# Kernel optimization log

Hardware: AMD Instinct MI355X
Metric: run time of the kernel (lower is better)

The kernel has to match this reference:

```python
import jax, jax.numpy as jnp
import numpy as np

ALPHA = 1.0
BETA = 0.5

B, N, E = 4096, 4096, 16384


def setup_inputs() -> dict:
    key = jax.random.key(0)
    k1, k2, k3, k4, k5 = jax.random.split(key, 5)
    outputs = jax.random.normal(k1, (B, N), dtype=jnp.float32)
    targets = jax.random.uniform(k2, (B, N), dtype=jnp.float32)
    # per-node level weight (equivalent to node_levels dict -> level_weights lookup)
    level_w = jax.random.uniform(k3, (N,), dtype=jnp.float32)
    edge_src = jax.random.randint(k4, (E,), 0, N, dtype=jnp.int32)  # parent i
    edge_dst = jax.random.randint(k5, (E,), 0, N, dtype=jnp.int32)  # child  j
    return {"outputs": outputs, "targets": targets, "level_w": level_w,
            "edge_src": edge_src, "edge_dst": edge_dst}


def reference(outputs, targets, level_w, edge_src, edge_dst):
    # BCEWithLogits, reduction='none': softplus(x) - x*t (numerically stable)
    bce = jax.nn.softplus(outputs) - outputs * targets          # [B, N]
    weighted_bce = bce * level_w[None, :]                        # [B, N]

    probs = jax.nn.sigmoid(outputs)                              # [B, N]
    # for each edge (i=parent, j=child): consistency[:, j] += relu(p[:, j] - p[:, i])
    diff = jax.nn.relu(probs[:, edge_dst] - probs[:, edge_src])  # [B, E]
    consistency = jnp.zeros_like(probs).at[:, edge_dst].add(diff)  # [B, N]

    return ALPHA * weighted_bce.mean() + BETA * consistency.mean()
```

## Files before the change

kernel.cpp:

```cpp
#include <hip/hip_runtime.h>
#include <math.h>


#define ALPHA_C 1.0f
#define BETA_C  0.5f

constexpr int B = 4096;
constexpr int N = 4096;
constexpr int E = 16384;
constexpr int THREADS = 1024;
constexpr int GRID = 256;
constexpr int R = 4;
constexpr int ROWS_PB = B / GRID;
constexpr int GPB = ROWS_PB / R;
constexpr int EPC = E / 4 / THREADS;

typedef _Float16 h4 __attribute__((ext_vector_type(4)));

__global__ __launch_bounds__(64) void init_out_kernel(float* out) {
    if (threadIdx.x == 0) out[0] = 0.0f;
}

__device__ __forceinline__ void fast_sig_sp(float x, float& p, float& sp) {
    float q = __expf(-fabsf(x));
    float d = 1.0f + q;
    float r = __builtin_amdgcn_rcpf(d);
    p  = (x >= 0.0f) ? r : q * r;
    sp = fmaxf(x, 0.0f) + __logf(d);
}

__global__ __launch_bounds__(THREADS, 4) void hier_loss_kernel(
    const float* __restrict__ outputs,
    const float* __restrict__ targets,
    const float* __restrict__ level_w,
    const int*   __restrict__ edge_src,
    const int*   __restrict__ edge_dst,
    float*       __restrict__ out)
{
    __shared__ h4 P[2][N];

    const int tid  = threadIdx.x;
    const int row0 = blockIdx.x * ROWS_PB;

    const float4* out4 = (const float4*)outputs;
    const float4* tgt4 = (const float4*)targets;
    const float4* lw4  = (const float4*)level_w;
    const int4*   es4  = (const int4*)edge_src;
    const int4*   ed4  = (const int4*)edge_dst;

    const float4 w = lw4[tid];
    const float wv[4] = {w.x, w.y, w.z, w.w};

    int4 se[EPC], de[EPC];
#pragma unroll
    for (int j = 0; j < EPC; ++j) {
        se[j] = es4[tid + j * THREADS];
        de[j] = ed4[tid + j * THREADS];
    }

    float s1 = 0.0f, s2 = 0.0f;
    float4 xs[R], ts[R];

#pragma unroll
    for (int r = 0; r < R; ++r) {
        const size_t idx = (size_t)(row0 + r) * (N / 4) + tid;
        xs[r] = out4[idx];
        ts[r] = tgt4[idx];
    }
    {
        h4 tmp[4];
#pragma unroll
        for (int r = 0; r < R; ++r) {
            const float xv[4] = {xs[r].x, xs[r].y, xs[r].z, xs[r].w};
            const float tv[4] = {ts[r].x, ts[r].y, ts[r].z, ts[r].w};
#pragma unroll
            for (int k = 0; k < 4; ++k) {
                float p, sp;
                fast_sig_sp(xv[k], p, sp);
                s1 = fmaf(wv[k], sp - xv[k] * tv[k], s1);
                tmp[k][r] = (_Float16)p;
            }
        }
#pragma unroll
        for (int k = 0; k < 4; ++k) P[0][4 * tid + k] = tmp[k];
    }
    __syncthreads();

#pragma unroll
    for (int kg = 0; kg < GPB; ++kg) {
        if (kg + 1 < GPB) {
#pragma unroll
            for (int r = 0; r < R; ++r) {
                const size_t idx = (size_t)(row0 + (kg + 1) * R + r) * (N / 4) + tid;
                xs[r] = out4[idx];
                ts[r] = tgt4[idx];
            }
        }
        __builtin_amdgcn_sched_barrier(0);

        {
            const h4* Pc = P[kg & 1];
            h4 acc0 = {0, 0, 0, 0};
            h4 acc1 = {0, 0, 0, 0};
            const h4 zero = {0, 0, 0, 0};
#pragma unroll
            for (int j = 0; j < EPC; ++j) {
                const int4 s = se[j];
                const int4 d = de[j];
                h4 a0 = Pc[s.x], c0 = Pc[d.x];
                h4 a1 = Pc[s.y], c1 = Pc[d.y];
                h4 a2 = Pc[s.z], c2 = Pc[d.z];
                h4 a3 = Pc[s.w], c3 = Pc[d.w];
                acc0 += __builtin_elementwise_max(c0 - a0, zero);
                acc1 += __builtin_elementwise_max(c1 - a1, zero);
                acc0 += __builtin_elementwise_max(c2 - a2, zero);
                acc1 += __builtin_elementwise_max(c3 - a3, zero);
            }
#pragma unroll
            for (int l = 0; l < 4; ++l) s2 += (float)acc0[l] + (float)acc1[l];
        }
        __builtin_amdgcn_sched_barrier(0);

        if (kg + 1 < GPB) {
            h4 tmp[4];
#pragma unroll
            for (int r = 0; r < R; ++r) {
                const float xv[4] = {xs[r].x, xs[r].y, xs[r].z, xs[r].w};
                const float tv[4] = {ts[r].x, ts[r].y, ts[r].z, ts[r].w};
#pragma unroll
                for (int k = 0; k < 4; ++k) {
                    float p, sp;
                    fast_sig_sp(xv[k], p, sp);
                    s1 = fmaf(wv[k], sp - xv[k] * tv[k], s1);
                    tmp[k][r] = (_Float16)p;
                }
            }
#pragma unroll
            for (int k = 0; k < 4; ++k) P[(kg + 1) & 1][4 * tid + k] = tmp[k];
        }
        __syncthreads();
    }

#pragma unroll
    for (int off = 32; off > 0; off >>= 1) {
        s1 += __shfl_down(s1, off, 64);
        s2 += __shfl_down(s2, off, 64);
    }
    float* red = (float*)P;
    const int wave = tid >> 6;
    const int lane = tid & 63;
    if (lane == 0) { red[wave] = s1; red[16 + wave] = s2; }
    __syncthreads();
    if (tid == 0) {
        float a = 0.0f, c = 0.0f;
#pragma unroll
        for (int v = 0; v < 16; ++v) { a += red[v]; c += red[16 + v]; }
        const float inv = 1.0f / ((float)B * (float)N);
        atomicAdd(out, (ALPHA_C * a + BETA_C * c) * inv);
    }
}

extern "C" void kernel_launch(void* const* d_in, const int* in_sizes, int n_in,
                              void* d_out, int out_size, void* d_ws, size_t ws_size,
                              hipStream_t stream) {
    const float* outputs = (const float*)d_in[0];
    const float* targets = (const float*)d_in[1];
    const float* level_w = (const float*)d_in[2];
    const int*   edge_src = (const int*)d_in[3];
    const int*   edge_dst = (const int*)d_in[4];
    float* out = (float*)d_out;

    init_out_kernel<<<1, 64, 0, stream>>>(out);
    hier_loss_kernel<<<GRID, THREADS, 0, stream>>>(outputs, targets, level_w,
                                                   edge_src, edge_dst, out);
}
```

Measured before the change: 155.1 us.

## Prefetch two row groups ahead and stage edge indices in LDS as u16

Deepens the global-load prefetch from one to two row groups by double-buffering the input registers. Edge indices move from per-thread registers into shared memory as 16-bit values, freeing VGPRs at the cost of extra LDS reads per edge batch. The __syncthreads calls become a manual lgkmcnt wait plus s_barrier so the barrier does not wait on outstanding global loads. The deeper prefetch and larger LDS footprint may reduce occupancy.

Result: slower. 160.3 us (+3.4%).

```diff
diff --git a/kernel.cpp b/kernel.cpp
--- a/kernel.cpp
+++ b/kernel.cpp
@@ -13,9 +13,10 @@
 constexpr int R = 4;
 constexpr int ROWS_PB = B / GRID;
 constexpr int GPB = ROWS_PB / R;
-constexpr int EPC = E / 4 / THREADS;
+constexpr int EPT4 = E / 4 / THREADS;
 
 typedef _Float16 h4 __attribute__((ext_vector_type(4)));
+typedef unsigned short us4 __attribute__((ext_vector_type(4)));
 
 __global__ __launch_bounds__(64) void init_out_kernel(float* out) {
     if (threadIdx.x == 0) out[0] = 0.0f;
@@ -38,6 +39,8 @@
     float*       __restrict__ out)
 {
     __shared__ h4 P[2][N];
+    __shared__ unsigned short IS[E];
+    __shared__ unsigned short ID[E];
 
     const int tid  = threadIdx.x;
     const int row0 = blockIdx.x * ROWS_PB;
@@ -47,32 +50,50 @@
     const float4* lw4  = (const float4*)level_w;
     const int4*   es4  = (const int4*)edge_src;
     const int4*   ed4  = (const int4*)edge_dst;
+    us4* IS4 = (us4*)IS;
+    us4* ID4 = (us4*)ID;
+
+    float s1 = 0.0f, s2 = 0.0f;
 
     const float4 w = lw4[tid];
+    int4 sei[EPT4], dei[EPT4];
+#pragma unroll
+    for (int j = 0; j < EPT4; ++j) {
+        sei[j] = es4[tid + j * THREADS];
+        dei[j] = ed4[tid + j * THREADS];
+    }
+    float4 xs[2][R], ts[2][R];
+#pragma unroll
+    for (int g = 0; g < 2; ++g)
+#pragma unroll
+    for (int r = 0; r < R; ++r) {
+        const size_t idx = (size_t)(row0 + g * R + r) * (N / 4) + tid;
+        xs[g][r] = out4[idx];
+        ts[g][r] = tgt4[idx];
+    }
+    __builtin_amdgcn_sched_barrier(0);
+
     const float wv[4] = {w.x, w.y, w.z, w.w};
 
-    int4 se[EPC], de[EPC];
 #pragma unroll
-    for (int j = 0; j < EPC; ++j) {
-        se[j] = es4[tid + j * THREADS];
-        de[j] = ed4[tid + j * THREADS];
+    for (int j = 0; j < EPT4; ++j) {
+        us4 ps = {(unsigned short)sei[j].x, (unsigned short)sei[j].y,
+                  (unsigned short)sei[j].z, (unsigned short)sei[j].w};
+        us4 pd = {(unsigned short)dei[j].x, (unsigned short)dei[j].y,
+                  (unsigned short)dei[j].z, (unsigned short)dei[j].w};
+        IS4[tid + j * THREADS] = ps;
+        ID4[tid + j * THREADS] = pd;
     }
+    __builtin_amdgcn_sched_barrier(0);
 
-    float s1 = 0.0f, s2 = 0.0f;
-    float4 xs[R], ts[R];
-
-#pragma unroll
-    for (int r = 0; r < R; ++r) {
-        const size_t idx = (size_t)(row0 + r) * (N / 4) + tid;
-        xs[r] = out4[idx];
-        ts[r] = tgt4[idx];
-    }
-    {
+    auto transform = [&](int slot, h4* Pb) {
         h4 tmp[4];
 #pragma unroll
         for (int r = 0; r < R; ++r) {
-            const float xv[4] = {xs[r].x, xs[r].y, xs[r].z, xs[r].w};
-            const float tv[4] = {ts[r].x, ts[r].y, ts[r].z, ts[r].w};
+            const float xv[4] = {xs[slot][r].x, xs[slot][r].y,
+                                 xs[slot][r].z, xs[slot][r].w};
+            const float tv[4] = {ts[slot][r].x, ts[slot][r].y,
+                                 ts[slot][r].z, ts[slot][r].w};
 #pragma unroll
             for (int k = 0; k < 4; ++k) {
                 float p, sp;
@@ -82,18 +103,24 @@
             }
         }
 #pragma unroll
-        for (int k = 0; k < 4; ++k) P[0][4 * tid + k] = tmp[k];
-    }
-    __syncthreads();
+        for (int k = 0; k < 4; ++k) Pb[4 * tid + k] = tmp[k];
+    };
+
+    transform(0, P[0]);
+    asm volatile("s_waitcnt lgkmcnt(0)" ::: "memory");
+    __builtin_amdgcn_s_barrier();
+    __builtin_amdgcn_sched_barrier(0);
 
 #pragma unroll
     for (int kg = 0; kg < GPB; ++kg) {
-        if (kg + 1 < GPB) {
+        if (kg + 2 < GPB) {
+            const int slot = kg & 1;
 #pragma unroll
             for (int r = 0; r < R; ++r) {
-                const size_t idx = (size_t)(row0 + (kg + 1) * R + r) * (N / 4) + tid;
-                xs[r] = out4[idx];
-                ts[r] = tgt4[idx];
+                const size_t idx =
+                    (size_t)(row0 + (kg + 2) * R + r) * (N / 4) + tid;
+                xs[slot][r] = out4[idx];
+                ts[slot][r] = tgt4[idx];
             }
         }
         __builtin_amdgcn_sched_barrier(0);
@@ -104,13 +131,13 @@
             h4 acc1 = {0, 0, 0, 0};
             const h4 zero = {0, 0, 0, 0};
 #pragma unroll
-            for (int j = 0; j < EPC; ++j) {
-                const int4 s = se[j];
-                const int4 d = de[j];
-                h4 a0 = Pc[s.x], c0 = Pc[d.x];
-                h4 a1 = Pc[s.y], c1 = Pc[d.y];
-                h4 a2 = Pc[s.z], c2 = Pc[d.z];
-                h4 a3 = Pc[s.w], c3 = Pc[d.w];
+            for (int j = 0; j < EPT4; ++j) {
+                const us4 s = IS4[tid + j * THREADS];
+                const us4 d = ID4[tid + j * THREADS];
+                h4 a0 = Pc[s[0]], c0 = Pc[d[0]];
+                h4 a1 = Pc[s[1]], c1 = Pc[d[1]];
+                h4 a2 = Pc[s[2]], c2 = Pc[d[2]];
+                h4 a3 = Pc[s[3]], c3 = Pc[d[3]];
                 acc0 += __builtin_elementwise_max(c0 - a0, zero);
                 acc1 += __builtin_elementwise_max(c1 - a1, zero);
                 acc0 += __builtin_elementwise_max(c2 - a2, zero);
@@ -121,24 +148,11 @@
         }
         __builtin_amdgcn_sched_barrier(0);
 
-        if (kg + 1 < GPB) {
-            h4 tmp[4];
-#pragma unroll
-            for (int r = 0; r < R; ++r) {
-                const float xv[4] = {xs[r].x, xs[r].y, xs[r].z, xs[r].w};
-                const float tv[4] = {ts[r].x, ts[r].y, ts[r].z, ts[r].w};
-#pragma unroll
-                for (int k = 0; k < 4; ++k) {
-                    float p, sp;
-                    fast_sig_sp(xv[k], p, sp);
-                    s1 = fmaf(wv[k], sp - xv[k] * tv[k], s1);
-                    tmp[k][r] = (_Float16)p;
-                }
-            }
-#pragma unroll
-            for (int k = 0; k < 4; ++k) P[(kg + 1) & 1][4 * tid + k] = tmp[k];
-        }
-        __syncthreads();
+        if (kg + 1 < GPB) transform((kg + 1) & 1, P[(kg + 1) & 1]);
+
+        asm volatile("s_waitcnt lgkmcnt(0)" ::: "memory");
+        __builtin_amdgcn_s_barrier();
+        __builtin_amdgcn_sched_barrier(0);
     }
 
 #pragma unroll
```
